# Kernel tuning notes

Measured on AMD Instinct MI355X. Metric: run time of the kernel, lower is better.

## Reference

```python
import jax, jax.numpy as jnp
import numpy as np

DIM = 1024
H = 16
HD = DIM // H  # 64
SCALE = HD ** -0.5
EPS = 1e-5


def setup_inputs() -> dict:
    key = jax.random.key(0)
    ks = jax.random.split(key, 8)
    B, N = 2, 2048
    x = jax.random.normal(ks[0], (B, N, DIM), dtype=jnp.float32)
    qkv_w = jax.random.normal(ks[1], (5 * DIM, DIM), dtype=jnp.float32) * (DIM ** -0.5)
    proj_w = jax.random.normal(ks[2], (DIM, DIM), dtype=jnp.float32) * (DIM ** -0.5)
    proj_b = jnp.zeros((DIM,), dtype=jnp.float32)
    lambda_q1 = jax.random.normal(ks[3], (HD,), dtype=jnp.float32) * 0.1
    lambda_k1 = jax.random.normal(ks[4], (HD,), dtype=jnp.float32) * 0.1
    lambda_q2 = jax.random.normal(ks[5], (HD,), dtype=jnp.float32) * 0.1
    lambda_k2 = jax.random.normal(ks[6], (HD,), dtype=jnp.float32) * 0.1
    return {"x": x, "qkv_w": qkv_w, "proj_w": proj_w, "proj_b": proj_b,
            "lambda_q1": lambda_q1, "lambda_k1": lambda_k1,
            "lambda_q2": lambda_q2, "lambda_k2": lambda_k2}


def reference(x, qkv_w, proj_w, proj_b, lambda_q1, lambda_k1, lambda_q2, lambda_k2):
    B, N, C = x.shape
    # qkv projection -> (5, B, H, N, hd)
    qkv = jnp.einsum('bnc,fc->bnf', x, qkv_w).reshape(B, N, 5, H, HD)
    qkv = jnp.transpose(qkv, (2, 0, 3, 1, 4))
    q1, q2, k1, k2, v = qkv[0], qkv[1], qkv[2], qkv[3], qkv[4]
    # dual attention score matrices (B, H, N, N)
    attn1 = jax.nn.softmax(jnp.einsum('bhqd,bhkd->bhqk', q1, k1) * SCALE, axis=-1)
    attn2 = jax.nn.softmax(jnp.einsum('bhqd,bhkd->bhqk', q2, k2) * SCALE, axis=-1)
    lambda_full = (jnp.exp(jnp.sum(lambda_q1 * lambda_k1))
                   - jnp.exp(jnp.sum(lambda_q2 * lambda_k2)) + 0.8)
    attn = attn1 - lambda_full * attn2
    out = jnp.einsum('bhqk,bhkd->bhqd', attn, v)  # (B,H,N,hd)
    out = jnp.transpose(out, (0, 2, 1, 3)).reshape(B, N, C)
    # RMSNorm (no affine) over last dim, then fixed scale (1 - 0.8)
    out = out * jax.lax.rsqrt(jnp.mean(out * out, axis=-1, keepdims=True) + EPS)
    out = out * (1.0 - 0.8)
    return jnp.einsum('bnc,oc->bno', out, proj_w) + proj_b
```

## Files before the change

kernel.cpp:

```cpp
#include <hip/hip_runtime.h>
#include <hip/hip_bf16.h>

#define SEQ   2048
#define BATCH 2
#define NHEAD 16
#define HDIM  64
#define CDIM  1024
#define QKV_F 5120
#define SCALE 0.125f
#define LOG2E 1.44269504f
#define EPSV  1e-5f

typedef __bf16 bf16;
typedef __bf16 bf16x4 __attribute__((ext_vector_type(4)));
typedef __bf16 bf16x8 __attribute__((ext_vector_type(8)));
typedef float  f32x4  __attribute__((ext_vector_type(4)));

#define MFMA16(a, b, c) __builtin_amdgcn_mfma_f32_16x16x32_bf16(a, b, c, 0, 0, 0)

__device__ __forceinline__ unsigned pkbf(float a, float b) {
    union { bf16 h[2]; unsigned u; } t;
    t.h[0] = (bf16)a; t.h[1] = (bf16)b;
    return t.u;
}
__device__ __forceinline__ unsigned short bfbits(float a) {
    union { bf16 h; unsigned short u; } t;
    t.h = (bf16)a;
    return t.u;
}
__device__ __forceinline__ void gload16(const void* g, void* l) {
    __builtin_amdgcn_global_load_lds(
        (const __attribute__((address_space(1))) unsigned int*)g,
        (__attribute__((address_space(3))) unsigned int*)l, 16, 0, 0);
}

__global__ __launch_bounds__(256) void cvt_bf16(
    const float* __restrict__ s, bf16* __restrict__ d)
{
    const int i = (blockIdx.x * 256 + threadIdx.x) * 8;
    float4 a = *(const float4*)(s + i);
    float4 b = *(const float4*)(s + i + 4);
    bf16x8 t;
    t[0] = (bf16)a.x; t[1] = (bf16)a.y; t[2] = (bf16)a.z; t[3] = (bf16)a.w;
    t[4] = (bf16)b.x; t[5] = (bf16)b.y; t[6] = (bf16)b.z; t[7] = (bf16)b.w;
    *(bf16x8*)(d + i) = t;
}

template <int EPI>
__global__ __launch_bounds__(256) void gemm_lds(
    const bf16* __restrict__ A, const bf16* __restrict__ Bw,
    const float* __restrict__ bias,
    bf16* __restrict__ outq, float* __restrict__ outp,
    int M, int Nn, int K)
{
    __shared__ __align__(16) bf16 As[128 * 64];
    __shared__ __align__(16) bf16 Bs[128 * 64];

    const int tid  = threadIdx.x;
    const int lane = tid & 63;
    const int wave = tid >> 6;
    const int wr = wave >> 1, wc = wave & 1;
    const int g = lane >> 4, fr = lane & 15;
    const int m0 = blockIdx.y * 128;
    const int n0 = blockIdx.x * 128;

    const int lrow = lane >> 3;
    const int lcol = (lane & 7) << 3;

    f32x4 acc[4][4];
#pragma unroll
    for (int m = 0; m < 4; ++m)
#pragma unroll
        for (int n = 0; n < 4; ++n) acc[m][n] = f32x4{0.f, 0.f, 0.f, 0.f};

    const int nkt = K >> 6;
    for (int kt = 0; kt < nkt; ++kt) {
        const int k0 = kt << 6;
        __syncthreads();
#pragma unroll
        for (int i = 0; i < 4; ++i) {
            const int chunk = wave * 4 + i;
            const int row = chunk * 8 + lrow;
            gload16(A + (size_t)(m0 + row) * K + k0 + lcol, As + chunk * 512);
            gload16(Bw + (size_t)(n0 + row) * K + k0 + lcol, Bs + chunk * 512);
        }
        __syncthreads();
#pragma unroll
        for (int ks = 0; ks < 2; ++ks) {
            bf16x8 af[4], bfr[4];
#pragma unroll
            for (int m = 0; m < 4; ++m)
                af[m] = *(const bf16x8*)(As + (wr * 64 + m * 16 + fr) * 64 + ks * 32 + g * 8);
#pragma unroll
            for (int n = 0; n < 4; ++n)
                bfr[n] = *(const bf16x8*)(Bs + (wc * 64 + n * 16 + fr) * 64 + ks * 32 + g * 8);
#pragma unroll
            for (int m = 0; m < 4; ++m)
#pragma unroll
                for (int n = 0; n < 4; ++n)
                    acc[m][n] = MFMA16(af[m], bfr[n], acc[m][n]);
        }
    }

#pragma unroll
    for (int m = 0; m < 4; ++m) {
#pragma unroll
        for (int n = 0; n < 4; ++n) {
            const int row0 = m0 + wr * 64 + m * 16 + g * 4;
            const int col  = n0 + wc * 64 + n * 16 + fr;
            if (EPI == 0) {
                const int bb = row0 >> 11, nn = row0 & (SEQ - 1);
                const int sI = col >> 10, rem = col & (CDIM - 1);
                const int hh = rem >> 6, dd = rem & 63;
                const size_t base = ((size_t)((sI * BATCH + bb) * NHEAD + hh)) << 17;
                if (sI == 4) {
                    ushort4 u;
                    u.x = bfbits(acc[m][n][0]);
                    u.y = bfbits(acc[m][n][1]);
                    u.z = bfbits(acc[m][n][2]);
                    u.w = bfbits(acc[m][n][3]);
                    *(ushort4*)(outq + base + ((size_t)dd << 11) + nn) = u;
                } else {
                    const float sc = (sI < 2) ? SCALE * LOG2E : 1.f;
#pragma unroll
                    for (int r = 0; r < 4; ++r)
                        outq[base + ((size_t)(nn + r) << 6) + dd] = (bf16)(acc[m][n][r] * sc);
                }
            } else {
#pragma unroll
                for (int r = 0; r < 4; ++r)
                    outp[(size_t)(row0 + r) * Nn + col] = acc[m][n][r] + bias[col];
            }
        }
    }
}

__global__ __launch_bounds__(256, 4) void diff_attn(
    const bf16* __restrict__ qkv,
    const float* __restrict__ lq1, const float* __restrict__ lk1,
    const float* __restrict__ lq2, const float* __restrict__ lk2,
    float* __restrict__ attn_out)
{
    __shared__ __align__(16) char K1s[8192];
    __shared__ __align__(16) char K2s[8192];
    __shared__ __align__(16) char Vts[8192];

    const int tid = threadIdx.x;
    const int lane = tid & 63, wave = tid >> 6;
    const int g = lane >> 4, fr = lane & 15;
    const int bh = blockIdx.x, b = bh >> 4, h = bh & 15;
    const int q0 = blockIdx.y * 64 + wave * 16;

    float ls1 = 0.f, ls2 = 0.f;
    for (int i = 0; i < HDIM; ++i) { ls1 += lq1[i] * lk1[i]; ls2 += lq2[i] * lk2[i]; }
    const float lam = __expf(ls1) - __expf(ls2) + 0.8f;

    const size_t HS = (size_t)SEQ * HDIM;
    const char* q1p = (const char*)(qkv + ((size_t)((0 * BATCH + b) * NHEAD + h)) * HS);
    const char* q2p = (const char*)(qkv + ((size_t)((1 * BATCH + b) * NHEAD + h)) * HS);
    const char* k1p = (const char*)(qkv + ((size_t)((2 * BATCH + b) * NHEAD + h)) * HS);
    const char* k2p = (const char*)(qkv + ((size_t)((3 * BATCH + b) * NHEAD + h)) * HS);
    const char* vtp = (const char*)(qkv + ((size_t)((4 * BATCH + b) * NHEAD + h)) * HS);

    bf16x8 qf1[2], qf2[2];
#pragma unroll
    for (int ks = 0; ks < 2; ++ks) {
        qf1[ks] = *(const bf16x8*)(q1p + (size_t)(q0 + fr) * 128 + ks * 64 + g * 16);
        qf2[ks] = *(const bf16x8*)(q2p + (size_t)(q0 + fr) * 128 + ks * 64 + g * 16);
    }

    f32x4 o1[4], o2[4];
#pragma unroll
    for (int d = 0; d < 4; ++d) { o1[d] = f32x4{0, 0, 0, 0}; o2[d] = f32x4{0, 0, 0, 0}; }
    float m1 = -1e30f, l1 = 0.f, m2 = -1e30f, l2 = 0.f;

    const int lrow8 = lane >> 3;
    const int scol  = ((lane & 7) ^ lrow8) << 4;
    const int vd = tid >> 2;
    const char* vsrc = vtp + (size_t)vd * (SEQ * 2);
    char* vdst = Vts + vd * 128;
    const int vswz = (vd & 7) << 4;

    auto qk_sm = [&](const char* Ks, const bf16x8* qf, f32x4* o,
                     float& mS, float& lS, unsigned* pw) {
        f32x4 s0{0, 0, 0, 0}, s1{0, 0, 0, 0}, s2{0, 0, 0, 0}, s3{0, 0, 0, 0};
        __builtin_amdgcn_s_setprio(1);
#pragma unroll
        for (int ks = 0; ks < 2; ++ks) {
            const int c = (ks * 64 + g * 16);
            bf16x8 k0 = *(const bf16x8*)(Ks + (0 * 16 + fr) * 128 + (c ^ ((fr & 7) << 4)));
            bf16x8 k1 = *(const bf16x8*)(Ks + (1 * 16 + fr) * 128 + (c ^ ((fr & 7) << 4)));
            bf16x8 k2 = *(const bf16x8*)(Ks + (2 * 16 + fr) * 128 + (c ^ ((fr & 7) << 4)));
            bf16x8 k3 = *(const bf16x8*)(Ks + (3 * 16 + fr) * 128 + (c ^ ((fr & 7) << 4)));
            s0 = MFMA16(k0, qf[ks], s0);
            s1 = MFMA16(k1, qf[ks], s1);
            s2 = MFMA16(k2, qf[ks], s2);
            s3 = MFMA16(k3, qf[ks], s3);
        }
        __builtin_amdgcn_s_setprio(0);
        f32x4 t01 = __builtin_elementwise_max(s0, s1);
        f32x4 t23 = __builtin_elementwise_max(s2, s3);
        f32x4 t = __builtin_elementwise_max(t01, t23);
        float pm = fmaxf(fmaxf(t[0], t[1]), fmaxf(t[2], t[3]));
        pm = fmaxf(pm, __shfl_xor(pm, 16));
        pm = fmaxf(pm, __shfl_xor(pm, 32));
        if (!__all(pm <= mS + 8.f * LOG2E)) {
            float mn = fmaxf(mS, pm);
            float alpha = __builtin_amdgcn_exp2f(mS - mn);
            lS *= alpha;
#pragma unroll
            for (int d = 0; d < 4; ++d) o[d] *= alpha;
            mS = mn;
        }
#pragma unroll
        for (int r = 0; r < 4; ++r) {
            s0[r] = __builtin_amdgcn_exp2f(s0[r] - mS);
            s1[r] = __builtin_amdgcn_exp2f(s1[r] - mS);
            s2[r] = __builtin_amdgcn_exp2f(s2[r] - mS);
            s3[r] = __builtin_amdgcn_exp2f(s3[r] - mS);
        }
        f32x4 u01 = (s0 + s1) + (s2 + s3);
        float rs = (u01[0] + u01[1]) + (u01[2] + u01[3]);
        rs += __shfl_xor(rs, 16);
        rs += __shfl_xor(rs, 32);
        lS += rs;
        pw[0] = pkbf(s0[0], s0[1]); pw[1] = pkbf(s0[2], s0[3]);
        pw[2] = pkbf(s1[0], s1[1]); pw[3] = pkbf(s1[2], s1[3]);
        pw[4] = pkbf(s2[0], s2[1]); pw[5] = pkbf(s2[2], s2[3]);
        pw[6] = pkbf(s3[0], s3[1]); pw[7] = pkbf(s3[2], s3[3]);
    };

    for (int kt = 0; kt < SEQ / 64; ++kt) {
        const int kvb = kt * 64;
        __syncthreads();
#pragma unroll
        for (int i = 0; i < 4; ++i) {
            const int c = wave * 4 + i;
            const int t = c >> 3, ch = c & 7;
            const char* kb = t ? k2p : k1p;
            gload16(kb + (size_t)(kvb + ch * 8 + lrow8) * 128 + scol,
                    (t ? K2s : K1s) + ch * 1024);
        }
        uint2 vv[4];
#pragma unroll
        for (int i = 0; i < 4; ++i) {
            const int u = (tid & 3) * 4 + i;
            const int G = u >> 3, gg = (u >> 1) & 3, jh = u & 1;
            const int kvrun = 8 * G + 4 * jh + gg;
            vv[i] = *(const uint2*)(vsrc + (size_t)(kvb + kvrun * 4) * 2);
        }
#pragma unroll
        for (int i = 0; i < 4; ++i) {
            const int u = (tid & 3) * 4 + i;
            *(uint2*)(vdst + ((u * 8) ^ vswz)) = vv[i];
        }
        __syncthreads();

        unsigned p1w[8], p2w[8];
        qk_sm(K1s, qf1, o1, m1, l1, p1w);
        qk_sm(K2s, qf2, o2, m2, l2, p2w);

        __builtin_amdgcn_s_setprio(1);
#pragma unroll
        for (int G = 0; G < 2; ++G) {
            union { unsigned u[4]; bf16x8 v; } pf1, pf2;
            pf1.u[0] = p1w[G * 4 + 0]; pf1.u[1] = p1w[G * 4 + 1];
            pf1.u[2] = p1w[G * 4 + 2]; pf1.u[3] = p1w[G * 4 + 3];
            pf2.u[0] = p2w[G * 4 + 0]; pf2.u[1] = p2w[G * 4 + 1];
            pf2.u[2] = p2w[G * 4 + 2]; pf2.u[3] = p2w[G * 4 + 3];
#pragma unroll
            for (int ds = 0; ds < 4; ++ds) {
                const int vrow = ds * 16 + fr;
                bf16x8 vf = *(const bf16x8*)(Vts + vrow * 128 +
                              ((G * 64 + g * 16) ^ ((vrow & 7) << 4)));
                o1[ds] = MFMA16(vf, pf1.v, o1[ds]);
                o2[ds] = MFMA16(vf, pf2.v, o2[ds]);
            }
        }
        __builtin_amdgcn_s_setprio(0);
    }

    const float i1 = 1.f / l1;
    const float i2 = lam / l2;
    float* op = attn_out + ((size_t)(b * SEQ + q0 + fr)) * CDIM + h * HDIM;
#pragma unroll
    for (int ds = 0; ds < 4; ++ds) {
        float4 o;
        o.x = o1[ds][0] * i1 - i2 * o2[ds][0];
        o.y = o1[ds][1] * i1 - i2 * o2[ds][1];
        o.z = o1[ds][2] * i1 - i2 * o2[ds][2];
        o.w = o1[ds][3] * i1 - i2 * o2[ds][3];
        *(float4*)(op + ds * 16 + g * 4) = o;
    }
}

__global__ __launch_bounds__(256) void rmsnorm_bf16(
    const float* __restrict__ in, bf16* __restrict__ out)
{
    __shared__ float red[4];
    const int row = blockIdx.x, tid = threadIdx.x;
    const float4 v = ((const float4*)(in + (size_t)row * CDIM))[tid];
    float ss = v.x * v.x + v.y * v.y + v.z * v.z + v.w * v.w;
#pragma unroll
    for (int m = 1; m < 64; m <<= 1) ss += __shfl_xor(ss, m);
    if ((tid & 63) == 0) red[tid >> 6] = ss;
    __syncthreads();
    float tot = red[0] + red[1] + red[2] + red[3];
    float sc = rsqrtf(tot * (1.f / CDIM) + EPSV) * 0.2f;
    bf16x4 o;
    o[0] = (bf16)(v.x * sc); o[1] = (bf16)(v.y * sc);
    o[2] = (bf16)(v.z * sc); o[3] = (bf16)(v.w * sc);
    ((bf16x4*)(out + (size_t)row * CDIM))[tid] = o;
}

extern "C" void kernel_launch(void* const* d_in, const int* in_sizes, int n_in,
                              void* d_out, int out_size, void* d_ws, size_t ws_size,
                              hipStream_t stream)
{
    (void)in_sizes; (void)n_in; (void)out_size; (void)ws_size;
    const float* x      = (const float*)d_in[0];
    const float* qkv_w  = (const float*)d_in[1];
    const float* proj_w = (const float*)d_in[2];
    const float* proj_b = (const float*)d_in[3];
    const float* lq1    = (const float*)d_in[4];
    const float* lk1    = (const float*)d_in[5];
    const float* lq2    = (const float*)d_in[6];
    const float* lk2    = (const float*)d_in[7];
    float* out = (float*)d_out;

    char* ws = (char*)d_ws;
    bf16*  qkv_t    = (bf16*)ws;
    bf16*  attn_b   = (bf16*)ws;
    float* attn_out = (float*)(ws + (size_t)40 * 1024 * 1024);
    bf16*  x_b      = (bf16*)(ws + (size_t)40 * 1024 * 1024);
    bf16*  qkvw_b   = (bf16*)(ws + (size_t)56 * 1024 * 1024);
    bf16*  projw_b  = (bf16*)(ws + (size_t)66 * 1024 * 1024);

    dim3 blk(256);
    cvt_bf16<<<dim3((BATCH * SEQ * CDIM) / 2048), blk, 0, stream>>>(x, x_b);
    cvt_bf16<<<dim3((QKV_F * CDIM) / 2048), blk, 0, stream>>>(qkv_w, qkvw_b);
    cvt_bf16<<<dim3((CDIM * CDIM) / 2048), blk, 0, stream>>>(proj_w, projw_b);
    gemm_lds<0><<<dim3(QKV_F / 128, (BATCH * SEQ) / 128), blk, 0, stream>>>(
        x_b, qkvw_b, nullptr, qkv_t, nullptr, BATCH * SEQ, QKV_F, CDIM);
    diff_attn<<<dim3(BATCH * NHEAD, SEQ / 64), blk, 0, stream>>>(
        qkv_t, lq1, lk1, lq2, lk2, attn_out);
    rmsnorm_bf16<<<dim3(BATCH * SEQ), blk, 0, stream>>>(attn_out, attn_b);
    gemm_lds<1><<<dim3(CDIM / 128, (BATCH * SEQ) / 128), blk, 0, stream>>>(
        attn_b, projw_b, proj_b, nullptr, out, BATCH * SEQ, CDIM, CDIM);
}
```

Measured before the change: 229.7 us.

## Double-buffer K/V tiles with async loads and pre-permuted V layout

The attention kernel now double-buffers the K1, K2 and V tiles in shared memory, issuing async global-to-LDS loads for the next tile while the current one is computed. That removes one barrier per iteration and hides load latency. The QKV GEMM epilogue writes V^T in a pre-permuted key order, so V can be staged with plain 16-byte direct loads instead of a register round-trip. Row sums are kept per lane and reduced once at the end. The larger shared-memory footprint lowers the occupancy target from 4 to 3 blocks.

```diff
diff --git a/kernel.cpp b/kernel.cpp
--- a/kernel.cpp
+++ b/kernel.cpp
@@ -114,12 +114,16 @@
                 const int hh = rem >> 6, dd = rem & 63;
                 const size_t base = ((size_t)((sI * BATCH + bb) * NHEAD + hh)) << 17;
                 if (sI == 4) {
-                    ushort4 u;
-                    u.x = bfbits(acc[m][n][0]);
-                    u.y = bfbits(acc[m][n][1]);
-                    u.z = bfbits(acc[m][n][2]);
-                    u.w = bfbits(acc[m][n][3]);
-                    *(ushort4*)(outq + base + ((size_t)dd << 11) + nn) = u;
+                    const int t4 = (nn >> 2) & 15;
+                    const int G = t4 >> 3, jh = (t4 >> 2) & 1, gg = t4 & 3;
+                    const int u = (G << 3) | (gg << 1) | jh;
+                    const int nnp = (nn & ~63) | (u << 2);
+                    ushort4 uu;
+                    uu.x = bfbits(acc[m][n][0]);
+                    uu.y = bfbits(acc[m][n][1]);
+                    uu.z = bfbits(acc[m][n][2]);
+                    uu.w = bfbits(acc[m][n][3]);
+                    *(ushort4*)(outq + base + ((size_t)dd << 11) + nnp) = uu;
                 } else {
                     const float sc = (sI < 2) ? SCALE * LOG2E : 1.f;
 #pragma unroll
@@ -135,15 +139,14 @@
     }
 }
 
-__global__ __launch_bounds__(256, 4) void diff_attn(
+__global__ __launch_bounds__(256, 3) void diff_attn(
     const bf16* __restrict__ qkv,
     const float* __restrict__ lq1, const float* __restrict__ lk1,
     const float* __restrict__ lq2, const float* __restrict__ lk2,
     float* __restrict__ attn_out)
 {
-    __shared__ __align__(16) char K1s[8192];
-    __shared__ __align__(16) char K2s[8192];
-    __shared__ __align__(16) char Vts[8192];
+    __shared__ __align__(16) char SM0[24576];
+    __shared__ __align__(16) char SM1[24576];
 
     const int tid = threadIdx.x;
     const int lane = tid & 63, wave = tid >> 6;
@@ -169,35 +172,47 @@
         qf2[ks] = *(const bf16x8*)(q2p + (size_t)(q0 + fr) * 128 + ks * 64 + g * 16);
     }
 
+    const f32x4 z4{0.f, 0.f, 0.f, 0.f};
     f32x4 o1[4], o2[4];
 #pragma unroll
-    for (int d = 0; d < 4; ++d) { o1[d] = f32x4{0, 0, 0, 0}; o2[d] = f32x4{0, 0, 0, 0}; }
-    float m1 = -1e30f, l1 = 0.f, m2 = -1e30f, l2 = 0.f;
+    for (int d = 0; d < 4; ++d) { o1[d] = z4; o2[d] = z4; }
+    f32x4 l1v = z4, l2v = z4;
+    float m1 = -1e30f, m2 = -1e30f;
 
     const int lrow8 = lane >> 3;
     const int scol  = ((lane & 7) ^ lrow8) << 4;
-    const int vd = tid >> 2;
-    const char* vsrc = vtp + (size_t)vd * (SEQ * 2);
-    char* vdst = Vts + vd * 128;
-    const int vswz = (vd & 7) << 4;
+    const int xw    = (fr & 7) << 4;
+
+    auto stage = [&](char* buf, int kvb) {
+#pragma unroll
+        for (int i = 0; i < 6; ++i) {
+            const int c = wave * 6 + i;
+            const int t = c >> 3, ch = c & 7;
+            const int row = ch * 8 + lrow8;
+            char* ldst = buf + t * 8192 + ch * 1024;
+            const char* src;
+            if (t == 0)      src = k1p + (size_t)(kvb + row) * 128 + scol;
+            else if (t == 1) src = k2p + (size_t)(kvb + row) * 128 + scol;
+            else             src = vtp + (size_t)row * (SEQ * 2) + (size_t)kvb * 2 + scol;
+            gload16(src, ldst);
+        }
+    };
 
     auto qk_sm = [&](const char* Ks, const bf16x8* qf, f32x4* o,
-                     float& mS, float& lS, unsigned* pw) {
-        f32x4 s0{0, 0, 0, 0}, s1{0, 0, 0, 0}, s2{0, 0, 0, 0}, s3{0, 0, 0, 0};
+                     float& mS, f32x4& lSv, unsigned* pw) {
+#define KRD(n, ks) (*(const bf16x8*)(Ks + ((n) * 16 + fr) * 128 + (((ks) * 64 + g * 16) ^ xw)))
+        f32x4 s0, s1, s2, s3;
         __builtin_amdgcn_s_setprio(1);
-#pragma unroll
-        for (int ks = 0; ks < 2; ++ks) {
-            const int c = (ks * 64 + g * 16);
-            bf16x8 k0 = *(const bf16x8*)(Ks + (0 * 16 + fr) * 128 + (c ^ ((fr & 7) << 4)));
-            bf16x8 k1 = *(const bf16x8*)(Ks + (1 * 16 + fr) * 128 + (c ^ ((fr & 7) << 4)));
-            bf16x8 k2 = *(const bf16x8*)(Ks + (2 * 16 + fr) * 128 + (c ^ ((fr & 7) << 4)));
-            bf16x8 k3 = *(const bf16x8*)(Ks + (3 * 16 + fr) * 128 + (c ^ ((fr & 7) << 4)));
-            s0 = MFMA16(k0, qf[ks], s0);
-            s1 = MFMA16(k1, qf[ks], s1);
-            s2 = MFMA16(k2, qf[ks], s2);
-            s3 = MFMA16(k3, qf[ks], s3);
-        }
+        s0 = MFMA16(KRD(0, 0), qf[0], z4);
+        s1 = MFMA16(KRD(1, 0), qf[0], z4);
+        s2 = MFMA16(KRD(2, 0), qf[0], z4);
+        s3 = MFMA16(KRD(3, 0), qf[0], z4);
+        s0 = MFMA16(KRD(0, 1), qf[1], s0);
+        s1 = MFMA16(KRD(1, 1), qf[1], s1);
+        s2 = MFMA16(KRD(2, 1), qf[1], s2);
+        s3 = MFMA16(KRD(3, 1), qf[1], s3);
         __builtin_amdgcn_s_setprio(0);
+#undef KRD
         f32x4 t01 = __builtin_elementwise_max(s0, s1);
         f32x4 t23 = __builtin_elementwise_max(s2, s3);
         f32x4 t = __builtin_elementwise_max(t01, t23);
@@ -207,7 +222,7 @@
         if (!__all(pm <= mS + 8.f * LOG2E)) {
             float mn = fmaxf(mS, pm);
             float alpha = __builtin_amdgcn_exp2f(mS - mn);
-            lS *= alpha;
+            lSv *= alpha;
 #pragma unroll
             for (int d = 0; d < 4; ++d) o[d] *= alpha;
             mS = mn;
@@ -219,47 +234,20 @@
             s2[r] = __builtin_amdgcn_exp2f(s2[r] - mS);
             s3[r] = __builtin_amdgcn_exp2f(s3[r] - mS);
         }
-        f32x4 u01 = (s0 + s1) + (s2 + s3);
-        float rs = (u01[0] + u01[1]) + (u01[2] + u01[3]);
-        rs += __shfl_xor(rs, 16);
-        rs += __shfl_xor(rs, 32);
-        lS += rs;
+        lSv += (s0 + s1) + (s2 + s3);
         pw[0] = pkbf(s0[0], s0[1]); pw[1] = pkbf(s0[2], s0[3]);
         pw[2] = pkbf(s1[0], s1[1]); pw[3] = pkbf(s1[2], s1[3]);
         pw[4] = pkbf(s2[0], s2[1]); pw[5] = pkbf(s2[2], s2[3]);
         pw[6] = pkbf(s3[0], s3[1]); pw[7] = pkbf(s3[2], s3[3]);
     };
 
-    for (int kt = 0; kt < SEQ / 64; ++kt) {
-        const int kvb = kt * 64;
-        __syncthreads();
-#pragma unroll
-        for (int i = 0; i < 4; ++i) {
-            const int c = wave * 4 + i;
-            const int t = c >> 3, ch = c & 7;
-            const char* kb = t ? k2p : k1p;
-            gload16(kb + (size_t)(kvb + ch * 8 + lrow8) * 128 + scol,
-                    (t ? K2s : K1s) + ch * 1024);
-        }
-        uint2 vv[4];
-#pragma unroll
-        for (int i = 0; i < 4; ++i) {
-            const int u = (tid & 3) * 4 + i;
-            const int G = u >> 3, gg = (u >> 1) & 3, jh = u & 1;
-            const int kvrun = 8 * G + 4 * jh + gg;
-            vv[i] = *(const uint2*)(vsrc + (size_t)(kvb + kvrun * 4) * 2);
-        }
-#pragma unroll
-        for (int i = 0; i < 4; ++i) {
-            const int u = (tid & 3) * 4 + i;
-            *(uint2*)(vdst + ((u * 8) ^ vswz)) = vv[i];
-        }
-        __syncthreads();
-
+    auto process = [&](const char* buf) {
+        const char* K1s = buf;
+        const char* K2s = buf + 8192;
+        const char* Vts = buf + 16384;
         unsigned p1w[8], p2w[8];
-        qk_sm(K1s, qf1, o1, m1, l1, p1w);
-        qk_sm(K2s, qf2, o2, m2, l2, p2w);
-
+        qk_sm(K1s, qf1, o1, m1, l1v, p1w);
+        qk_sm(K2s, qf2, o2, m2, l2v, p2w);
         __builtin_amdgcn_s_setprio(1);
 #pragma unroll
         for (int G = 0; G < 2; ++G) {
@@ -278,7 +266,22 @@
             }
         }
         __builtin_amdgcn_s_setprio(0);
-    }
+    };
+
+    stage(SM0, 0);
+    for (int kt = 0; kt < SEQ / 64; kt += 2) {
+        __syncthreads();
+        stage(SM1, (kt + 1) * 64);
+        process(SM0);
+        __syncthreads();
+        if (kt + 2 < SEQ / 64) stage(SM0, (kt + 2) * 64);
+        process(SM1);
+    }
+
+    float l1 = (l1v[0] + l1v[1]) + (l1v[2] + l1v[3]);
+    float l2 = (l2v[0] + l2v[1]) + (l2v[2] + l2v[3]);
+    l1 += __shfl_xor(l1, 16); l1 += __shfl_xor(l1, 32);
+    l2 += __shfl_xor(l2, 16); l2 += __shfl_xor(l2, 32);
 
     const float i1 = 1.f / l1;
     const float i2 = lam / l2;
```

After: 318.9 us. +38.9%, slower.
